# Optimization experiments

Measured on AMD Instinct MI355X. Metric: run time of the kernel, lower is better.

Reference implementation:

```python
import jax, jax.numpy as jnp
import numpy as np

B, A, C, H, W = 16, 5, 512, 16, 16


def _affine_grid(theta, Hh, Ww):
    # torch F.affine_grid, align_corners=False (default). theta: [2,3]
    xs = (2.0 * jnp.arange(Ww, dtype=jnp.float32) + 1.0) / Ww - 1.0  # [W]
    ys = (2.0 * jnp.arange(Hh, dtype=jnp.float32) + 1.0) / Hh - 1.0  # [H]
    gx = theta[0, 0] * xs[None, :] + theta[0, 1] * ys[:, None] + theta[0, 2]  # [H,W]
    gy = theta[1, 0] * xs[None, :] + theta[1, 1] * ys[:, None] + theta[1, 2]  # [H,W]
    return gx, gy


def _grid_sample(img, gx, gy):
    # torch F.grid_sample, bilinear, padding_mode='zeros', align_corners=False
    # img: [C,H,W]; gx,gy: [H,W] normalized coords
    C_, Hh, Ww = img.shape
    ix = ((gx + 1.0) * Ww - 1.0) * 0.5
    iy = ((gy + 1.0) * Hh - 1.0) * 0.5
    x0 = jnp.floor(ix); y0 = jnp.floor(iy)
    x1 = x0 + 1.0;      y1 = y0 + 1.0
    wx1 = ix - x0; wx0 = 1.0 - wx1
    wy1 = iy - y0; wy0 = 1.0 - wy1

    def gather(xi, yi):
        inb = (xi >= 0) & (xi < Ww) & (yi >= 0) & (yi < Hh)
        xc = jnp.clip(xi, 0, Ww - 1).astype(jnp.int32)
        yc = jnp.clip(yi, 0, Hh - 1).astype(jnp.int32)
        return img[:, yc, xc] * inb[None].astype(img.dtype)  # [C,H,W]

    return (gather(x0, y0) * (wx0 * wy0)[None] + gather(x1, y0) * (wx1 * wy0)[None]
          + gather(x0, y1) * (wx0 * wy1)[None] + gather(x1, y1) * (wx1 * wy1)[None])


def _warp(nb_feat, nb_warp):
    # nb_feat: [C,H,W] neighbor feature; nb_warp: [4,4] pose matrix
    zero = jnp.zeros((), dtype=jnp.float32)
    one = jnp.ones((), dtype=jnp.float32)
    theta_rot = jnp.stack([
        jnp.stack([nb_warp[0, 0], nb_warp[0, 1], zero]),
        jnp.stack([nb_warp[1, 0], nb_warp[1, 1], zero])])  # [2,3]
    gx_r, gy_r = _affine_grid(theta_rot, H, W)
    feat_rot = _grid_sample(nb_feat, gx_r, gy_r)
    x_trans = 4.0 * nb_warp[0, 3] / 128.0
    y_trans = -(4.0 * nb_warp[1, 3]) / 128.0
    theta_trans = jnp.stack([
        jnp.stack([one, zero, x_trans]),
        jnp.stack([zero, one, y_trans])])
    gx_t, gy_t = _affine_grid(theta_trans, H, W)
    return _grid_sample(feat_rot, gx_t, gy_t)  # [C,H,W]


def _fuse_one(local_b, trans_b, n):
    # local_b: [A,C,H,W], trans_b: [A,A,4,4], n: scalar num_agent
    # pair[i,j] = warp of agent j's feature into agent i's frame
    pair = jax.vmap(lambda t_i: jax.vmap(_warp)(local_b, t_i))(trans_b)  # [A,A,C,H,W]
    idx = jnp.arange(A)
    mask = (idx[:, None] != idx[None, :]) & (idx[:, None] < n) & (idx[None, :] < n)
    return local_b + jnp.einsum('ij,ijchw->ichw', mask.astype(local_b.dtype), pair)


def setup_inputs() -> dict:
    key = jax.random.key(0)
    k1, k2, k3, k4 = jax.random.split(key, 4)
    feat_maps = jax.random.normal(k1, (A * B, C, H, W), dtype=jnp.float32)
    # realistic near-rigid pose matrices: rotation block + translation column
    ang = jax.random.uniform(k2, (B, A, A), minval=-0.5, maxval=0.5)
    tr = jax.random.normal(k3, (B, A, A, 2), dtype=jnp.float32) * 8.0
    tm = jnp.zeros((B, A, A, 4, 4), dtype=jnp.float32)
    tm = tm.at[..., 0, 0].set(jnp.cos(ang)).at[..., 0, 1].set(-jnp.sin(ang))
    tm = tm.at[..., 1, 0].set(jnp.sin(ang)).at[..., 1, 1].set(jnp.cos(ang))
    tm = tm.at[..., 0, 3].set(tr[..., 0]).at[..., 1, 3].set(tr[..., 1])
    tm = tm.at[..., 2, 2].set(1.0).at[..., 3, 3].set(1.0)
    num_agent = jax.random.randint(k4, (B, A), 1, 6, dtype=jnp.int64) if jax.config.jax_enable_x64 else jax.random.randint(k4, (B, A), 1, 6, dtype=jnp.int32)
    return {"feat_maps": feat_maps, "trans_matrices": tm, "num_agent_tensor": num_agent}


def reference(feat_maps, trans_matrices, num_agent_tensor):
    # feat_maps is agent-major blocks of size B (feat_maps[B*i:B*(i+1)] is agent i)
    local = feat_maps.reshape(A, B, C, H, W).transpose(1, 0, 2, 3, 4)  # [B,A,C,H,W]
    fused = jax.vmap(_fuse_one)(local, trans_matrices, num_agent_tensor[:, 0])
    # agents2batch: concat agents along batch dim -> [A*B,C,H,W]
    return fused.transpose(1, 0, 2, 3, 4).reshape(A * B, C, H, W)
```

## Files before the change

kernel.cpp:

```cpp
#include <hip/hip_runtime.h>

#define NB 16
#define NA 5
#define NC 512
#define HW 256
#define NBLK 2048
#define NTOT 5120

typedef _Float16 h8 __attribute__((ext_vector_type(8)));

static __device__ __forceinline__ h8 splat8(float v) {
    const _Float16 h = (_Float16)v;
    h8 r = {h, h, h, h, h, h, h, h};
    return r;
}

static __device__ __forceinline__ float rfl(float v) {
    return __builtin_bit_cast(float,
        __builtin_amdgcn_readfirstlane(__builtin_bit_cast(int, v)));
}

struct Item {
    int i, b, c0, n;
    bool work;
    float own[8];
    float nb[4][8];
    float tr[4][6];
};

static __device__ __forceinline__ Item prefetch_item(
        const float* __restrict__ feat, const float* __restrict__ trans,
        const int* __restrict__ numa, int idx, int p) {
    Item it;
    const int g = idx & 63;
    const int r = idx >> 6;
    it.i = r % NA;
    it.b = r / NA;
    it.c0 = g << 3;
    it.n = numa[it.b * NA];
    it.work = (it.i < it.n) && (it.n > 1);
    const float* own = feat + ((it.i * NB + it.b) * NC + it.c0) * HW + p;
#pragma unroll
    for (int k = 0; k < 8; ++k) it.own[k] = own[k * HW];
    if (it.work) {
#pragma unroll
        for (int jj = 0; jj < 4; ++jj) {
            const int j = jj + (jj >= it.i);
            if (j < it.n) {
                const float* tw = trans + (((it.b * NA) + it.i) * NA + j) * 16;
                it.tr[jj][0] = rfl(tw[0]);
                it.tr[jj][1] = rfl(tw[1]);
                it.tr[jj][2] = rfl(tw[3]);
                it.tr[jj][3] = rfl(tw[4]);
                it.tr[jj][4] = rfl(tw[5]);
                it.tr[jj][5] = rfl(tw[7]);
                const float* src = feat + ((j * NB + it.b) * NC + it.c0) * HW + p;
#pragma unroll
                for (int k = 0; k < 8; ++k) it.nb[jj][k] = src[k * HW];
            }
        }
    }
    return it;
}

__global__ __launch_bounds__(256, 4) void fafmimo_twophase_kernel(
    const float* __restrict__ feat,
    const float* __restrict__ trans,
    const int*   __restrict__ numa,
    float*       __restrict__ out)
{
    __shared__ h8 lds_nb[4][HW];
    __shared__ h8 lds_rot[4][HW];

    const int p = threadIdx.x;
    const int x = p & 15, y = p >> 4;
    const float fx = (float)x - 7.5f;
    const float fy = (float)y - 7.5f;
    bool dirty = false;

    int idx = blockIdx.x;
    Item cur = prefetch_item(feat, trans, numa, idx, p);

    while (true) {
        if (cur.work) {
            if (dirty) __syncthreads();
#pragma unroll
            for (int jj = 0; jj < 4; ++jj) {
                const int j = jj + (jj >= cur.i);
                if (j < cur.n) {
                    h8 v;
#pragma unroll
                    for (int k = 0; k < 8; ++k) v[k] = (_Float16)cur.nb[jj][k];
                    lds_nb[jj][p] = v;
                }
            }
            __syncthreads();
            dirty = true;
        }

        const int nidx = idx + NBLK;
        const bool more = nidx < NTOT;
        Item nxt;
        if (more) nxt = prefetch_item(feat, trans, numa, nidx, p);

        float acc[8];
#pragma unroll
        for (int k = 0; k < 8; ++k) acc[k] = cur.own[k];

        if (cur.work) {
#pragma unroll
            for (int jj = 0; jj < 4; ++jj) {
                const int j = jj + (jj >= cur.i);
                if (j < cur.n) {
                    const float bx = cur.tr[jj][0] * fx + cur.tr[jj][1] * fy + 7.5f;
                    const float by = cur.tr[jj][3] * fx + cur.tr[jj][4] * fy + 7.5f;
                    const float fbx = floorf(bx), fby = floorf(by);
                    const int ix = (int)fbx, iy = (int)fby;
                    const float wx1 = bx - fbx, wy1 = by - fby;
                    const float mx0 = (ix     >= 0 && ix     < 16) ? 1.0f - wx1 : 0.0f;
                    const float mx1 = (ix + 1 >= 0 && ix + 1 < 16) ? wx1 : 0.0f;
                    const float my0 = (iy     >= 0 && iy     < 16) ? 1.0f - wy1 : 0.0f;
                    const float my1 = (iy + 1 >= 0 && iy + 1 < 16) ? wy1 : 0.0f;
                    const int cx0 = min(max(ix, 0), 15), cx1 = min(max(ix + 1, 0), 15);
                    const int cy0 = min(max(iy, 0), 15), cy1 = min(max(iy + 1, 0), 15);
                    const h8 v00 = lds_nb[jj][cy0 * 16 + cx0];
                    const h8 v01 = lds_nb[jj][cy0 * 16 + cx1];
                    const h8 v10 = lds_nb[jj][cy1 * 16 + cx0];
                    const h8 v11 = lds_nb[jj][cy1 * 16 + cx1];
                    lds_rot[jj][p] =
                          v00 * splat8(mx0 * my0) + v01 * splat8(mx1 * my0)
                        + v10 * splat8(mx0 * my1) + v11 * splat8(mx1 * my1);
                }
            }
            __syncthreads();

#pragma unroll
            for (int jj = 0; jj < 4; ++jj) {
                const int j = jj + (jj >= cur.i);
                if (j < cur.n) {
                    const float dx = 0.25f * cur.tr[jj][2];
                    const float dy = -0.25f * cur.tr[jj][5];
                    const float fdx = floorf(dx), fdy = floorf(dy);
                    const float tx1 = dx - fdx, tx0 = 1.0f - tx1;
                    const float ty1 = dy - fdy, ty0 = 1.0f - ty1;
                    const int ox = x + (int)fdx;
                    const int oy = y + (int)fdy;
                    const bool inx0 = (ox     >= 0) && (ox     < 16);
                    const bool inx1 = (ox + 1 >= 0) && (ox + 1 < 16);
                    const bool iny0 = (oy     >= 0) && (oy     < 16);
                    const bool iny1 = (oy + 1 >= 0) && (oy + 1 < 16);
                    const float w00 = (inx0 && iny0) ? tx0 * ty0 : 0.0f;
                    const float w10 = (inx1 && iny0) ? tx1 * ty0 : 0.0f;
                    const float w01 = (inx0 && iny1) ? tx0 * ty1 : 0.0f;
                    const float w11 = (inx1 && iny1) ? tx1 * ty1 : 0.0f;
                    const int cx0 = min(max(ox, 0), 15), cx1 = min(max(ox + 1, 0), 15);
                    const int cy0 = min(max(oy, 0), 15), cy1 = min(max(oy + 1, 0), 15);
                    const h8 t00 = lds_rot[jj][cy0 * 16 + cx0];
                    const h8 t01 = lds_rot[jj][cy0 * 16 + cx1];
                    const h8 t10 = lds_rot[jj][cy1 * 16 + cx0];
                    const h8 t11 = lds_rot[jj][cy1 * 16 + cx1];
                    const h8 s = t00 * splat8(w00) + t01 * splat8(w10)
                               + t10 * splat8(w01) + t11 * splat8(w11);
#pragma unroll
                    for (int k = 0; k < 8; ++k) acc[k] += (float)s[k];
                }
            }
        }

        float* dst = out + ((cur.i * NB + cur.b) * NC + cur.c0) * HW + p;
#pragma unroll
        for (int k = 0; k < 8; ++k) dst[k * HW] = acc[k];

        if (!more) break;
        cur = nxt;
        idx = nidx;
    }
}

extern "C" void kernel_launch(void* const* d_in, const int* in_sizes, int n_in,
                              void* d_out, int out_size, void* d_ws, size_t ws_size,
                              hipStream_t stream) {
    const float* feat  = (const float*)d_in[0];
    const float* trans = (const float*)d_in[1];
    const int*   numa  = (const int*)d_in[2];
    float* out = (float*)d_out;

    fafmimo_twophase_kernel<<<dim3(NBLK), dim3(256), 0, stream>>>(
        feat, trans, numa, out);
}
```

Baseline: 96.82 us.

## Process all agents per block to reuse neighbor features from LDS

Restructures the kernel so each block handles one batch and channel group for all five agents, loading each agent's feature slab once into shared memory. Every target agent then warps neighbors from that shared copy instead of re-reading them from global memory. This removes redundant global reads of neighbor features but drops the persistent prefetch pipeline and halves the grid, adding register pressure and per-agent barriers.

```diff
diff --git a/kernel.cpp b/kernel.cpp
--- a/kernel.cpp
+++ b/kernel.cpp
@@ -4,8 +4,6 @@
 #define NA 5
 #define NC 512
 #define HW 256
-#define NBLK 2048
-#define NTOT 5120
 
 typedef _Float16 h8 __attribute__((ext_vector_type(8)));
 
@@ -20,100 +18,62 @@
         __builtin_amdgcn_readfirstlane(__builtin_bit_cast(int, v)));
 }
 
-struct Item {
-    int i, b, c0, n;
-    bool work;
-    float own[8];
-    float nb[4][8];
-    float tr[4][6];
-};
-
-static __device__ __forceinline__ Item prefetch_item(
-        const float* __restrict__ feat, const float* __restrict__ trans,
-        const int* __restrict__ numa, int idx, int p) {
-    Item it;
-    const int g = idx & 63;
-    const int r = idx >> 6;
-    it.i = r % NA;
-    it.b = r / NA;
-    it.c0 = g << 3;
-    it.n = numa[it.b * NA];
-    it.work = (it.i < it.n) && (it.n > 1);
-    const float* own = feat + ((it.i * NB + it.b) * NC + it.c0) * HW + p;
-#pragma unroll
-    for (int k = 0; k < 8; ++k) it.own[k] = own[k * HW];
-    if (it.work) {
-#pragma unroll
-        for (int jj = 0; jj < 4; ++jj) {
-            const int j = jj + (jj >= it.i);
-            if (j < it.n) {
-                const float* tw = trans + (((it.b * NA) + it.i) * NA + j) * 16;
-                it.tr[jj][0] = rfl(tw[0]);
-                it.tr[jj][1] = rfl(tw[1]);
-                it.tr[jj][2] = rfl(tw[3]);
-                it.tr[jj][3] = rfl(tw[4]);
-                it.tr[jj][4] = rfl(tw[5]);
-                it.tr[jj][5] = rfl(tw[7]);
-                const float* src = feat + ((j * NB + it.b) * NC + it.c0) * HW + p;
-#pragma unroll
-                for (int k = 0; k < 8; ++k) it.nb[jj][k] = src[k * HW];
-            }
-        }
-    }
-    return it;
-}
-
-__global__ __launch_bounds__(256, 4) void fafmimo_twophase_kernel(
+__global__ __launch_bounds__(256, 4) void fafmimo_agentblock_kernel(
     const float* __restrict__ feat,
     const float* __restrict__ trans,
     const int*   __restrict__ numa,
     float*       __restrict__ out)
 {
-    __shared__ h8 lds_nb[4][HW];
+    __shared__ h8 lds_nb[NA][HW];
     __shared__ h8 lds_rot[4][HW];
 
     const int p = threadIdx.x;
     const int x = p & 15, y = p >> 4;
     const float fx = (float)x - 7.5f;
     const float fy = (float)y - 7.5f;
-    bool dirty = false;
 
-    int idx = blockIdx.x;
-    Item cur = prefetch_item(feat, trans, numa, idx, p);
+    const int idx = blockIdx.x;
+    const int b  = idx >> 6;
+    const int c0 = (idx & 63) << 3;
+    const int n  = numa[b * NA];
 
-    while (true) {
-        if (cur.work) {
-            if (dirty) __syncthreads();
+    float slab[NA][8];
+#pragma unroll
+    for (int a = 0; a < NA; ++a) {
+        const float* src = feat + ((a * NB + b) * NC + c0) * HW + p;
+#pragma unroll
+        for (int k = 0; k < 8; ++k) slab[a][k] = src[k * HW];
+    }
+
+#pragma unroll
+    for (int a = 0; a < NA; ++a) {
+        if (a < n) {
+            h8 v;
+#pragma unroll
+            for (int k = 0; k < 8; ++k) v[k] = (_Float16)slab[a][k];
+            lds_nb[a][p] = v;
+        }
+    }
+    __syncthreads();
+
+    const bool anyPairs = (n > 1);
+
+#pragma unroll
+    for (int i = 0; i < NA; ++i) {
+        float acc[8];
+#pragma unroll
+        for (int k = 0; k < 8; ++k) acc[k] = slab[i][k];
+
+        if (anyPairs && i < n) {
 #pragma unroll
             for (int jj = 0; jj < 4; ++jj) {
-                const int j = jj + (jj >= cur.i);
-                if (j < cur.n) {
-                    h8 v;
-#pragma unroll
-                    for (int k = 0; k < 8; ++k) v[k] = (_Float16)cur.nb[jj][k];
-                    lds_nb[jj][p] = v;
-                }
-            }
-            __syncthreads();
-            dirty = true;
-        }
-
-        const int nidx = idx + NBLK;
-        const bool more = nidx < NTOT;
-        Item nxt;
-        if (more) nxt = prefetch_item(feat, trans, numa, nidx, p);
-
-        float acc[8];
-#pragma unroll
-        for (int k = 0; k < 8; ++k) acc[k] = cur.own[k];
-
-        if (cur.work) {
-#pragma unroll
-            for (int jj = 0; jj < 4; ++jj) {
-                const int j = jj + (jj >= cur.i);
-                if (j < cur.n) {
-                    const float bx = cur.tr[jj][0] * fx + cur.tr[jj][1] * fy + 7.5f;
-                    const float by = cur.tr[jj][3] * fx + cur.tr[jj][4] * fy + 7.5f;
+                const int j = jj + (jj >= i);
+                if (j < n) {
+                    const float* tw = trans + (((b * NA) + i) * NA + j) * 16;
+                    const float r00 = rfl(tw[0]), r01 = rfl(tw[1]);
+                    const float r10 = rfl(tw[4]), r11 = rfl(tw[5]);
+                    const float bx = r00 * fx + r01 * fy + 7.5f;
+                    const float by = r10 * fx + r11 * fy + 7.5f;
                     const float fbx = floorf(bx), fby = floorf(by);
                     const int ix = (int)fbx, iy = (int)fby;
                     const float wx1 = bx - fbx, wy1 = by - fby;
@@ -123,10 +83,10 @@
                     const float my1 = (iy + 1 >= 0 && iy + 1 < 16) ? wy1 : 0.0f;
                     const int cx0 = min(max(ix, 0), 15), cx1 = min(max(ix + 1, 0), 15);
                     const int cy0 = min(max(iy, 0), 15), cy1 = min(max(iy + 1, 0), 15);
-                    const h8 v00 = lds_nb[jj][cy0 * 16 + cx0];
-                    const h8 v01 = lds_nb[jj][cy0 * 16 + cx1];
-                    const h8 v10 = lds_nb[jj][cy1 * 16 + cx0];
-                    const h8 v11 = lds_nb[jj][cy1 * 16 + cx1];
+                    const h8 v00 = lds_nb[j][cy0 * 16 + cx0];
+                    const h8 v01 = lds_nb[j][cy0 * 16 + cx1];
+                    const h8 v10 = lds_nb[j][cy1 * 16 + cx0];
+                    const h8 v11 = lds_nb[j][cy1 * 16 + cx1];
                     lds_rot[jj][p] =
                           v00 * splat8(mx0 * my0) + v01 * splat8(mx1 * my0)
                         + v10 * splat8(mx0 * my1) + v11 * splat8(mx1 * my1);
@@ -136,10 +96,11 @@
 
 #pragma unroll
             for (int jj = 0; jj < 4; ++jj) {
-                const int j = jj + (jj >= cur.i);
-                if (j < cur.n) {
-                    const float dx = 0.25f * cur.tr[jj][2];
-                    const float dy = -0.25f * cur.tr[jj][5];
+                const int j = jj + (jj >= i);
+                if (j < n) {
+                    const float* tw = trans + (((b * NA) + i) * NA + j) * 16;
+                    const float dx =  0.25f * rfl(tw[3]);
+                    const float dy = -0.25f * rfl(tw[7]);
                     const float fdx = floorf(dx), fdy = floorf(dy);
                     const float tx1 = dx - fdx, tx0 = 1.0f - tx1;
                     const float ty1 = dy - fdy, ty0 = 1.0f - ty1;
@@ -165,15 +126,12 @@
                     for (int k = 0; k < 8; ++k) acc[k] += (float)s[k];
                 }
             }
+            __syncthreads();
         }
 
-        float* dst = out + ((cur.i * NB + cur.b) * NC + cur.c0) * HW + p;
+        float* dst = out + ((i * NB + b) * NC + c0) * HW + p;
 #pragma unroll
         for (int k = 0; k < 8; ++k) dst[k * HW] = acc[k];
-
-        if (!more) break;
-        cur = nxt;
-        idx = nidx;
     }
 }
 
@@ -185,6 +143,6 @@
     const int*   numa  = (const int*)d_in[2];
     float* out = (float*)d_out;
 
-    fafmimo_twophase_kernel<<<dim3(NBLK), dim3(256), 0, stream>>>(
+    fafmimo_agentblock_kernel<<<dim3(NB * 64), dim3(256), 0, stream>>>(
         feat, trans, numa, out);
 }
```

Result: slower. 102.9 us (+6.3%).
